# Kernel tuning notes

Measured on AMD Instinct MI355X. Metric: run time of the kernel, lower is better.

Reference implementation:

```python
import jax, jax.numpy as jnp
import numpy as np

NUM_HEADS = 12


def setup_inputs() -> dict:
    key = jax.random.key(0)
    k0, k1, k2 = jax.random.split(key, 3)
    B, N, C = 32, 864, 768  # N = 2*t_h*t_w + s_h*s_w = 288 + 576
    x = jax.random.normal(k0, (B, N, C), dtype=jnp.float32)
    W_qkv = jax.random.normal(k1, (C, 3 * C), dtype=jnp.float32) * 0.02
    W_proj = jax.random.normal(k2, (C, C), dtype=jnp.float32) * 0.02
    b_proj = jnp.zeros((C,), dtype=jnp.float32)
    return {"x": x, "W_qkv": W_qkv, "W_proj": W_proj, "b_proj": b_proj,
            "t_h": 12, "t_w": 12, "s_h": 24, "s_w": 24}


def reference(x, W_qkv, W_proj, b_proj, t_h, t_w, s_h, s_w):
    B, N, C = x.shape
    H = NUM_HEADS
    d = C // H
    scale = d ** -0.5
    # qkv projection (no bias), shape [3, B, H, N, d]
    qkv = (x @ W_qkv).reshape(B, N, 3, H, d).transpose(2, 0, 3, 1, 4)
    q, k, v = qkv[0], qkv[1], qkv[2]
    Tt = 2 * t_h * t_w            # temporal (template) query tokens = 288
    Ts = s_h * s_w                # spatial (search) query tokens = 576
    Mt = 2 * ((t_h + 1) // 2) ** 2  # sub-sampled temporal kv tokens = 72
    Ms = (s_h * s_w) // 4           # sub-sampled spatial kv tokens = 144
    q_t, q_s = q[:, :, :Tt], q[:, :, Tt:Tt + Ts]
    k_t, k_s = k[:, :, :Mt], k[:, :, Mt:Mt + Ms]
    v_t, v_s = v[:, :, :Mt], v[:, :, Mt:Mt + Ms]
    # temporal queries attend spatial keys/values
    a_t = jax.nn.softmax(jnp.einsum('bhqd,bhkd->bhqk', q_t, k_s) * scale, axis=-1)
    x_t = jnp.einsum('bhqk,bhkd->bhqd', a_t, v_s).transpose(0, 2, 1, 3).reshape(B, Tt, C)
    # spatial queries attend temporal keys/values
    a_s = jax.nn.softmax(jnp.einsum('bhqd,bhkd->bhqk', q_s, k_t) * scale, axis=-1)
    x_s = jnp.einsum('bhqk,bhkd->bhqd', a_s, v_t).transpose(0, 2, 1, 3).reshape(B, Ts, C)
    out = jnp.concatenate([x_t, x_s], axis=1)  # [B, N, C]
    return out @ W_proj + b_proj
```

## Files before the change

### kernel.cpp

```cpp
#include <hip/hip_runtime.h>
#include <hip/hip_bf16.h>

typedef __attribute__((ext_vector_type(8))) short short8;
typedef __attribute__((ext_vector_type(4))) float floatx4;

#define MFMA16(a, b, c) __builtin_amdgcn_mfma_f32_16x16x32_bf16((a), (b), (c), 0, 0, 0)

static constexpr int Bb = 32, Nn = 864, Cc = 768, Hh = 12;
static constexpr int Mm = Bb * Nn;
static constexpr int KVROWS = 256;

__device__ __forceinline__ void gload_lds16(const __hip_bfloat16* g, __hip_bfloat16* l) {
    __builtin_amdgcn_global_load_lds((const __attribute__((address_space(1))) void*)g,
                                     (__attribute__((address_space(3))) void*)l, 16, 0, 0);
}

static constexpr int CVT_BLKS = (Mm * Cc / 4) / 256;
static constexpr int TQKV_BLKS = (3 * Cc / 32) * (Cc / 32);
static constexpr int TPROJ_BLKS = (Cc / 32) * (Cc / 32);

__global__ __launch_bounds__(256) void prep_kernel(const float* __restrict__ x,
                                                   const float* __restrict__ Wqkv,
                                                   const float* __restrict__ Wproj,
                                                   __hip_bfloat16* __restrict__ xb,
                                                   __hip_bfloat16* __restrict__ WqkvT,
                                                   __hip_bfloat16* __restrict__ WprojT) {
    __shared__ float tile[32][33];
    const int bx = blockIdx.x;
    if (bx < CVT_BLKS) {
        const int i = bx * 256 + threadIdx.x;
        const float4 v = ((const float4*)x)[i];
        __hip_bfloat16 o[4] = {__float2bfloat16(v.x), __float2bfloat16(v.y),
                               __float2bfloat16(v.z), __float2bfloat16(v.w)};
        ((uint2*)xb)[i] = *(const uint2*)o;
        return;
    }
    const float* in;
    __hip_bfloat16* out;
    int R, C, bid;
    if (bx < CVT_BLKS + TQKV_BLKS) {
        bid = bx - CVT_BLKS; in = Wqkv; out = WqkvT; R = Cc; C = 3 * Cc;
    } else {
        bid = bx - CVT_BLKS - TQKV_BLKS; in = Wproj; out = WprojT; R = Cc; C = Cc;
    }
    const int c0 = (bid % (C / 32)) * 32, r0 = (bid / (C / 32)) * 32;
    const int tx = threadIdx.x & 31, ty = threadIdx.x >> 5;
#pragma unroll
    for (int i = 0; i < 32; i += 8)
        tile[ty + i][tx] = in[(size_t)(r0 + ty + i) * C + c0 + tx];
    __syncthreads();
#pragma unroll
    for (int i = 0; i < 32; i += 8)
        out[(size_t)(c0 + ty + i) * R + r0 + tx] = __float2bfloat16(tile[tx][ty + i]);
}

static constexpr int QBLKS = 6 * (Mm / 128);
static constexpr int KVBLKS = 12 * (Bb * KVROWS / 128);
static constexpr int QKV_NWG = QBLKS + KVBLKS;

__global__ __launch_bounds__(256) void gemm_qkv(const __hip_bfloat16* __restrict__ A,
                                                const __hip_bfloat16* __restrict__ WqkvT,
                                                __hip_bfloat16* __restrict__ Qbuf,
                                                __hip_bfloat16* __restrict__ Kbuf,
                                                __hip_bfloat16* __restrict__ VTbuf) {
    __shared__ __align__(16) char SMEM[32768];
    __hip_bfloat16* As = (__hip_bfloat16*)SMEM;
    __hip_bfloat16* Bs = As + 8192;

    const int braw = (int)blockIdx.x;
    const int sid = (braw & 7) * (QKV_NWG / 8) + (braw >> 3);

    int arow0, orow0, btrow, ncol0, bb = 0, keybase = 0;
    __hip_bfloat16* Out;
    int Nout;
    bool vmode = false;
    if (sid < QBLKS) {
        const int nt = sid % 6, mt = sid / 6;
        arow0 = mt * 128; orow0 = arow0;
        btrow = nt * 128; ncol0 = nt * 128;
        Out = Qbuf; Nout = Cc;
    } else {
        const int s = sid - QBLKS;
        const int nt = s % 12, mt = s / 12;
        bb = mt >> 1; keybase = (mt & 1) << 7;
        arow0 = bb * Nn + keybase;
        btrow = Cc + nt * 128;
        if (nt < 6) {
            orow0 = bb * KVROWS + keybase; ncol0 = nt * 128;
            Out = Kbuf; Nout = Cc;
        } else {
            vmode = true; ncol0 = (nt - 6) * 128;
            Out = nullptr; Nout = 0; orow0 = 0;
        }
    }

    const int t = threadIdx.x;
    const int lane = t & 63, wave = t >> 6;
    const int wm = (wave >> 1) * 64, wn = (wave & 1) * 64;
    const int ln = lane & 15, quad = lane >> 4;

    floatx4 acc[4][4] = {};

    const int r0 = t >> 2;
    const int cst = (t & 3) * 8;
    const __hip_bfloat16* Ag = A + (size_t)(arow0 + r0) * Cc + cst;
    const __hip_bfloat16* Bg = WqkvT + (size_t)(btrow + r0) * Cc + cst;
    const size_t rowskip = (size_t)64 * Cc;

    for (int k0 = 0; k0 < Cc; k0 += 64) {
        gload_lds16(Ag + k0,                &As[t * 8]);
        gload_lds16(Ag + k0 + rowskip,      &As[2048 + t * 8]);
        gload_lds16(Ag + k0 + 32,           &As[4096 + t * 8]);
        gload_lds16(Ag + k0 + 32 + rowskip, &As[6144 + t * 8]);
        gload_lds16(Bg + k0,                &Bs[t * 8]);
        gload_lds16(Bg + k0 + rowskip,      &Bs[2048 + t * 8]);
        gload_lds16(Bg + k0 + 32,           &Bs[4096 + t * 8]);
        gload_lds16(Bg + k0 + 32 + rowskip, &Bs[6144 + t * 8]);
        __syncthreads();

#pragma unroll
        for (int s = 0; s < 2; s++) {
            short8 af[4], bfr[4];
#pragma unroll
            for (int i = 0; i < 4; i++)
                af[i] = *(const short8*)&As[s * 4096 + (wm + i * 16 + ln) * 32 + quad * 8];
#pragma unroll
            for (int j = 0; j < 4; j++)
                bfr[j] = *(const short8*)&Bs[s * 4096 + (wn + j * 16 + ln) * 32 + quad * 8];
#pragma unroll
            for (int i = 0; i < 4; i++)
#pragma unroll
                for (int j = 0; j < 4; j++)
                    acc[i][j] = MFMA16(af[i], bfr[j], acc[i][j]);
        }
        __syncthreads();
    }

    if (!vmode) {
#pragma unroll
        for (int j = 0; j < 4; j++) {
            const int n = ncol0 + wn + j * 16 + ln;
#pragma unroll
            for (int i = 0; i < 4; i++) {
                const int mrow = orow0 + wm + i * 16 + quad * 4;
#pragma unroll
                for (int r = 0; r < 4; r++)
                    Out[(size_t)(mrow + r) * Nout + n] = __float2bfloat16(acc[i][j][r]);
            }
        }
        return;
    }

    __hip_bfloat16* T = (__hip_bfloat16*)SMEM;
#pragma unroll
    for (int pass = 0; pass < 2; pass++) {
        if ((wave & 1) == pass) {
#pragma unroll
            for (int j = 0; j < 4; j++) {
                const int ddl = j * 16 + ln;
#pragma unroll
                for (int i = 0; i < 4; i++) {
                    const int key = wm + i * 16 + quad * 4;
                    const __hip_bfloat162 lo =
                        __float22bfloat162_rn(make_float2(acc[i][j][0], acc[i][j][1]));
                    const __hip_bfloat162 hi =
                        __float22bfloat162_rn(make_float2(acc[i][j][2], acc[i][j][3]));
                    uint2 pk = make_uint2(*(const unsigned int*)&lo,
                                          *(const unsigned int*)&hi);
                    *(uint2*)&T[ddl * 136 + key] = pk;
                }
            }
        }
        __syncthreads();
#pragma unroll
        for (int it = 0; it < 4; it++) {
            const int ldd = it * 16 + (t >> 4);
            const int kk = (t & 15) * 8;
            const short8 v = *(const short8*)&T[ldd * 136 + kk];
            *(short8*)&VTbuf[(size_t)(bb * Cc + ncol0 + pass * 64 + ldd) * KVROWS +
                             keybase + kk] = v;
        }
        if (pass == 0) __syncthreads();
    }
}

__global__ __launch_bounds__(256) void gemm_proj(const __hip_bfloat16* __restrict__ A,
                                                 const __hip_bfloat16* __restrict__ BT,
                                                 float* __restrict__ Cout,
                                                 const float* __restrict__ bias) {
    __shared__ __align__(16) __hip_bfloat16 As[8192];
    __shared__ __align__(16) __hip_bfloat16 Bs[8192];
    const int gx = (int)gridDim.x;
    const int nwg = gx * (int)gridDim.y;
    const int braw = (int)blockIdx.y * gx + (int)blockIdx.x;
    const int sid = (braw & 7) * (nwg >> 3) + (braw >> 3);
    const int mt = sid / gx, nt = sid - mt * gx;
    const int m0 = mt << 7, n0 = nt * 128;
    const int t = threadIdx.x;
    const int lane = t & 63, wave = t >> 6;
    const int wm = (wave >> 1) * 64, wn = (wave & 1) * 64;
    const int ln = lane & 15, quad = lane >> 4;

    floatx4 acc[4][4] = {};
    const int r0 = t >> 2, cst = (t & 3) * 8;
    const __hip_bfloat16* Ag = A + (size_t)(m0 + r0) * Cc + cst;
    const __hip_bfloat16* Bg = BT + (size_t)(n0 + r0) * Cc + cst;
    const size_t rowskip = (size_t)64 * Cc;

    for (int k0 = 0; k0 < Cc; k0 += 64) {
        gload_lds16(Ag + k0,                &As[t * 8]);
        gload_lds16(Ag + k0 + rowskip,      &As[2048 + t * 8]);
        gload_lds16(Ag + k0 + 32,           &As[4096 + t * 8]);
        gload_lds16(Ag + k0 + 32 + rowskip, &As[6144 + t * 8]);
        gload_lds16(Bg + k0,                &Bs[t * 8]);
        gload_lds16(Bg + k0 + rowskip,      &Bs[2048 + t * 8]);
        gload_lds16(Bg + k0 + 32,           &Bs[4096 + t * 8]);
        gload_lds16(Bg + k0 + 32 + rowskip, &Bs[6144 + t * 8]);
        __syncthreads();
#pragma unroll
        for (int s = 0; s < 2; s++) {
            short8 af[4], bfr[4];
#pragma unroll
            for (int i = 0; i < 4; i++)
                af[i] = *(const short8*)&As[s * 4096 + (wm + i * 16 + ln) * 32 + quad * 8];
#pragma unroll
            for (int j = 0; j < 4; j++)
                bfr[j] = *(const short8*)&Bs[s * 4096 + (wn + j * 16 + ln) * 32 + quad * 8];
#pragma unroll
            for (int i = 0; i < 4; i++)
#pragma unroll
                for (int j = 0; j < 4; j++)
                    acc[i][j] = MFMA16(af[i], bfr[j], acc[i][j]);
        }
        __syncthreads();
    }
#pragma unroll
    for (int j = 0; j < 4; j++) {
        const int n = n0 + wn + j * 16 + ln;
        const float bv = bias[n];
#pragma unroll
        for (int i = 0; i < 4; i++) {
            const int mrow = m0 + wm + i * 16 + quad * 4;
#pragma unroll
            for (int r = 0; r < 4; r++)
                Cout[(size_t)(mrow + r) * Cc + n] = acc[i][j][r] + bv;
        }
    }
}

template <int L, int QOFF, int KVOFF, int NCH>
__device__ __forceinline__ void attn_pair(const __hip_bfloat16* __restrict__ qb,
                                          const __hip_bfloat16* __restrict__ kb,
                                          const __hip_bfloat16* __restrict__ vtb,
                                          __hip_bfloat16* __restrict__ attn,
                                          int p, int h, int b) {
    const int lane = threadIdx.x & 63;
    const int ln = lane & 15, quad = lane >> 4;

    const __hip_bfloat16* kbase = kb + (size_t)(b * KVROWS + KVOFF) * Cc + h * 64;
    const __hip_bfloat16* vtbase = vtb + (size_t)(b * Cc + h * 64) * KVROWS + KVOFF;

    const int qt0 = 2 * p;
    const __hip_bfloat16* qrowA =
        qb + (size_t)(b * Nn + QOFF + qt0 * 16 + ln) * Cc + h * 64;
    const __hip_bfloat16* qrowB = qrowA + (size_t)16 * Cc;
    const short8 aqA0 = *(const short8*)(qrowA + quad * 8);
    const short8 aqA1 = *(const short8*)(qrowA + 32 + quad * 8);
    const short8 aqB0 = *(const short8*)(qrowB + quad * 8);
    const short8 aqB1 = *(const short8*)(qrowB + 32 + quad * 8);

    float dsA = 0.0f, dsB = 0.0f;
    floatx4 accA[4] = {}, accB[4] = {};
    constexpr float CSC = 0.18033688011112042f;

#pragma unroll
    for (int ch = 0; ch < NCH; ch++) {
        unsigned int pkA[2][2] = {}, pkB[2][2] = {};
#pragma unroll
        for (int ti2 = 0; ti2 < 2; ti2++) {
            const int ti = ch * 2 + ti2;
            if (ti * 16 >= L) continue;
            const __hip_bfloat16* krow = kbase + (size_t)(ti * 16 + ln) * Cc;
            const short8 k0 = *(const short8*)(krow + quad * 8);
            const short8 k1 = *(const short8*)(krow + 32 + quad * 8);
            floatx4 sA = {0.f, 0.f, 0.f, 0.f}, sB = {0.f, 0.f, 0.f, 0.f};
            sA = MFMA16(k0, aqA0, sA);
            sA = MFMA16(k1, aqA1, sA);
            sB = MFMA16(k0, aqB0, sB);
            sB = MFMA16(k1, aqB1, sB);
            float pA[4], pB[4];
#pragma unroll
            for (int r = 0; r < 4; r++) {
                float eA = exp2f(sA[r] * CSC);
                float eB = exp2f(sB[r] * CSC);
                if (ti * 16 + 16 > L) {
                    if (ti * 16 + quad * 4 + r >= L) { eA = 0.0f; eB = 0.0f; }
                }
                pA[r] = eA; dsA += eA;
                pB[r] = eB; dsB += eB;
            }
            {
                const __hip_bfloat162 lo = __float22bfloat162_rn(make_float2(pA[0], pA[1]));
                const __hip_bfloat162 hi = __float22bfloat162_rn(make_float2(pA[2], pA[3]));
                pkA[ti2][0] = *(const unsigned int*)&lo;
                pkA[ti2][1] = *(const unsigned int*)&hi;
            }
            {
                const __hip_bfloat162 lo = __float22bfloat162_rn(make_float2(pB[0], pB[1]));
                const __hip_bfloat162 hi = __float22bfloat162_rn(make_float2(pB[2], pB[3]));
                pkB[ti2][0] = *(const unsigned int*)&lo;
                pkB[ti2][1] = *(const unsigned int*)&hi;
            }
        }
        const int srcA = ln + ((quad & 1) << 5);
        const int srcB = srcA + 16;
        const bool hi2 = quad >= 2;
        union { unsigned int u[4]; short8 v; } pfA, pfB;
        {
            const unsigned int c0 = (unsigned int)__shfl((int)pkA[0][0], srcA);
            const unsigned int c1 = (unsigned int)__shfl((int)pkA[0][1], srcA);
            const unsigned int c2 = (unsigned int)__shfl((int)pkA[0][0], srcB);
            const unsigned int c3 = (unsigned int)__shfl((int)pkA[0][1], srcB);
            const unsigned int d0 = (unsigned int)__shfl((int)pkA[1][0], srcA);
            const unsigned int d1 = (unsigned int)__shfl((int)pkA[1][1], srcA);
            const unsigned int d2 = (unsigned int)__shfl((int)pkA[1][0], srcB);
            const unsigned int d3 = (unsigned int)__shfl((int)pkA[1][1], srcB);
            pfA.u[0] = hi2 ? d0 : c0;
            pfA.u[1] = hi2 ? d1 : c1;
            pfA.u[2] = hi2 ? d2 : c2;
            pfA.u[3] = hi2 ? d3 : c3;
        }
        {
            const unsigned int c0 = (unsigned int)__shfl((int)pkB[0][0], srcA);
            const unsigned int c1 = (unsigned int)__shfl((int)pkB[0][1], srcA);
            const unsigned int c2 = (unsigned int)__shfl((int)pkB[0][0], srcB);
            const unsigned int c3 = (unsigned int)__shfl((int)pkB[0][1], srcB);
            const unsigned int d0 = (unsigned int)__shfl((int)pkB[1][0], srcA);
            const unsigned int d1 = (unsigned int)__shfl((int)pkB[1][1], srcA);
            const unsigned int d2 = (unsigned int)__shfl((int)pkB[1][0], srcB);
            const unsigned int d3 = (unsigned int)__shfl((int)pkB[1][1], srcB);
            pfB.u[0] = hi2 ? d0 : c0;
            pfB.u[1] = hi2 ? d1 : c1;
            pfB.u[2] = hi2 ? d2 : c2;
            pfB.u[3] = hi2 ? d3 : c3;
        }
#pragma unroll
        for (int j = 0; j < 4; j++) {
            const short8 vt =
                *(const short8*)&vtbase[(size_t)(j * 16 + ln) * KVROWS + ch * 32 + quad * 8];
            accA[j] = MFMA16(vt, pfA.v, accA[j]);
            accB[j] = MFMA16(vt, pfB.v, accB[j]);
        }
    }

    dsA += __shfl_xor(dsA, 16); dsA += __shfl_xor(dsA, 32);
    dsB += __shfl_xor(dsB, 16); dsB += __shfl_xor(dsB, 32);
    const float invA = 1.0f / dsA, invB = 1.0f / dsB;

    const size_t orowA = (size_t)(b * Nn + QOFF + qt0 * 16 + ln) * Cc + h * 64;
    const size_t orowB = orowA + (size_t)16 * Cc;
#pragma unroll
    for (int j = 0; j < 4; j++) {
        {
            const __hip_bfloat162 lo =
                __float22bfloat162_rn(make_float2(accA[j][0] * invA, accA[j][1] * invA));
            const __hip_bfloat162 hi =
                __float22bfloat162_rn(make_float2(accA[j][2] * invA, accA[j][3] * invA));
            uint2 o = make_uint2(*(const unsigned int*)&lo, *(const unsigned int*)&hi);
            *(uint2*)&attn[orowA + j * 16 + quad * 4] = o;
        }
        {
            const __hip_bfloat162 lo =
                __float22bfloat162_rn(make_float2(accB[j][0] * invB, accB[j][1] * invB));
            const __hip_bfloat162 hi =
                __float22bfloat162_rn(make_float2(accB[j][2] * invB, accB[j][3] * invB));
            uint2 o = make_uint2(*(const unsigned int*)&lo, *(const unsigned int*)&hi);
            *(uint2*)&attn[orowB + j * 16 + quad * 4] = o;
        }
    }
}

static constexpr int ATTN_BLKS = (384 * 27) / 4;

__global__ __launch_bounds__(256) void attn_fused(const __hip_bfloat16* __restrict__ qb,
                                                  const __hip_bfloat16* __restrict__ kb,
                                                  const __hip_bfloat16* __restrict__ vtb,
                                                  __hip_bfloat16* __restrict__ attn) {
    const int rid = (int)blockIdx.x;
    const int vid = (rid & 7) * (ATTN_BLKS / 8) + (rid >> 3);
    const int g = vid * 4 + (threadIdx.x >> 6);
    const int bh = g / 27, slot = g - bh * 27;
    const int h = bh % 12, b = bh / 12;
    if (slot < 9)
        attn_pair<144, 0, 72, 5>(qb, kb, vtb, attn, slot, h, b);
    else
        attn_pair<72, 288, 0, 3>(qb, kb, vtb, attn, slot - 9, h, b);
}

extern "C" void kernel_launch(void* const* d_in, const int* in_sizes, int n_in,
                              void* d_out, int out_size, void* d_ws, size_t ws_size,
                              hipStream_t stream) {
    const float* x     = (const float*)d_in[0];
    const float* Wqkv  = (const float*)d_in[1];
    const float* Wproj = (const float*)d_in[2];
    const float* bproj = (const float*)d_in[3];
    float* out = (float*)d_out;

    char* ws = (char*)d_ws;
    __hip_bfloat16* xb     = (__hip_bfloat16*)ws;
    __hip_bfloat16* WqkvT  = (__hip_bfloat16*)(ws + 42467328);
    __hip_bfloat16* WprojT = (__hip_bfloat16*)(ws + 46006272);
    __hip_bfloat16* Qbuf   = (__hip_bfloat16*)(ws + 47185920);
    __hip_bfloat16* Kbuf   = (__hip_bfloat16*)(ws + 89653248);
    __hip_bfloat16* VTbuf  = (__hip_bfloat16*)(ws + 102236160);
    __hip_bfloat16* attn   = (__hip_bfloat16*)ws;

    prep_kernel<<<CVT_BLKS + TQKV_BLKS + TPROJ_BLKS, 256, 0, stream>>>(x, Wqkv, Wproj, xb,
                                                                       WqkvT, WprojT);
    gemm_qkv<<<QKV_NWG, 256, 0, stream>>>(xb, WqkvT, Qbuf, Kbuf, VTbuf);
    attn_fused<<<ATTN_BLKS, 256, 0, stream>>>(Qbuf, Kbuf, VTbuf, attn);
    gemm_proj<<<dim3(Cc / 128, Mm / 128), 256, 0, stream>>>(attn, WprojT, out, bproj);
}
```

Before: 345.0 us.

## Stage V-transpose tile in LDS per (batch,head) block, one query tile per wave

The attention kernel now gives each block a single (batch, head) pair plus a chunk of query tiles. The block cooperatively loads that head's transposed V slice into LDS with a rotated, padded layout to avoid bank conflicts, and each wave then processes one 16-row query tile instead of two. This replaces repeated uncoalesced global V reads with LDS reads, but adds a barrier and an LDS footprint, and some waves exit idle in the last chunk. Both the QKV GEMM and the attention kernel also get a minimum-occupancy launch bound of 5, which may constrain register allocation.

```diff
diff --git a/kernel.cpp b/kernel.cpp
--- a/kernel.cpp
+++ b/kernel.cpp
@@ -58,11 +58,11 @@
 static constexpr int KVBLKS = 12 * (Bb * KVROWS / 128);
 static constexpr int QKV_NWG = QBLKS + KVBLKS;
 
-__global__ __launch_bounds__(256) void gemm_qkv(const __hip_bfloat16* __restrict__ A,
-                                                const __hip_bfloat16* __restrict__ WqkvT,
-                                                __hip_bfloat16* __restrict__ Qbuf,
-                                                __hip_bfloat16* __restrict__ Kbuf,
-                                                __hip_bfloat16* __restrict__ VTbuf) {
+__global__ __launch_bounds__(256, 5) void gemm_qkv(const __hip_bfloat16* __restrict__ A,
+                                                   const __hip_bfloat16* __restrict__ WqkvT,
+                                                   __hip_bfloat16* __restrict__ Qbuf,
+                                                   __hip_bfloat16* __restrict__ Kbuf,
+                                                   __hip_bfloat16* __restrict__ VTbuf) {
     __shared__ __align__(16) char SMEM[32768];
     __hip_bfloat16* As = (__hip_bfloat16*)SMEM;
     __hip_bfloat16* Bs = As + 8192;
@@ -248,153 +248,133 @@
     }
 }
 
-template <int L, int QOFF, int KVOFF, int NCH>
-__device__ __forceinline__ void attn_pair(const __hip_bfloat16* __restrict__ qb,
+template <int L, int QOFF, int KVOFF, int NQT, int NCH>
+__device__ __forceinline__ void attn_part(const __hip_bfloat16* __restrict__ qb,
                                           const __hip_bfloat16* __restrict__ kb,
                                           const __hip_bfloat16* __restrict__ vtb,
                                           __hip_bfloat16* __restrict__ attn,
-                                          int p, int h, int b) {
-    const int lane = threadIdx.x & 63;
+                                          int qc, int h, int b,
+                                          __hip_bfloat16* VTs) {
+    constexpr int KPAD = NCH * 32;
+    constexpr int NB8 = KPAD / 8;
+    constexpr int VSTR = KPAD + 8;
+    const int t = threadIdx.x, lane = t & 63;
     const int ln = lane & 15, quad = lane >> 4;
 
     const __hip_bfloat16* kbase = kb + (size_t)(b * KVROWS + KVOFF) * Cc + h * 64;
-    const __hip_bfloat16* vtbase = vtb + (size_t)(b * Cc + h * 64) * KVROWS + KVOFF;
-
-    const int qt0 = 2 * p;
-    const __hip_bfloat16* qrowA =
-        qb + (size_t)(b * Nn + QOFF + qt0 * 16 + ln) * Cc + h * 64;
-    const __hip_bfloat16* qrowB = qrowA + (size_t)16 * Cc;
-    const short8 aqA0 = *(const short8*)(qrowA + quad * 8);
-    const short8 aqA1 = *(const short8*)(qrowA + 32 + quad * 8);
-    const short8 aqB0 = *(const short8*)(qrowB + quad * 8);
-    const short8 aqB1 = *(const short8*)(qrowB + 32 + quad * 8);
-
-    float dsA = 0.0f, dsB = 0.0f;
-    floatx4 accA[4] = {}, accB[4] = {};
+    const __hip_bfloat16* vtbase =
+        vtb + (size_t)(b * Cc + h * 64) * KVROWS + KVOFF;
+
+    for (int c = t; c < 64 * NB8; c += 256) {
+        const int dd = c / NB8, kbk = c - dd * NB8;
+        const int colp8 = (kbk + dd) % NB8;
+        uint4 val = make_uint4(0u, 0u, 0u, 0u);
+        if (kbk * 8 < L)
+            val = *(const uint4*)(vtbase + (size_t)dd * KVROWS + kbk * 8);
+        *(uint4*)&VTs[dd * VSTR + colp8 * 8] = val;
+    }
+    __syncthreads();
+
+    const int qt = qc * 4 + (t >> 6);
+    if (qt >= NQT) return;
+
+    const __hip_bfloat16* qrow = qb + (size_t)(b * Nn + QOFF + qt * 16 + ln) * Cc + h * 64;
+    const short8 aq0 = *(const short8*)(qrow + quad * 8);
+    const short8 aq1 = *(const short8*)(qrow + 32 + quad * 8);
+
+    int ddm[4];
+#pragma unroll
+    for (int j = 0; j < 4; j++) ddm[j] = (j * 16 + ln) % NB8;
+
+    float dsum = 0.0f;
+    floatx4 acco[4] = {};
     constexpr float CSC = 0.18033688011112042f;
 
 #pragma unroll
     for (int ch = 0; ch < NCH; ch++) {
-        unsigned int pkA[2][2] = {}, pkB[2][2] = {};
+        unsigned int pk[2][2];
 #pragma unroll
         for (int ti2 = 0; ti2 < 2; ti2++) {
             const int ti = ch * 2 + ti2;
-            if (ti * 16 >= L) continue;
+            if (ti * 16 >= L) {
+                pk[ti2][0] = 0u; pk[ti2][1] = 0u;
+                continue;
+            }
             const __hip_bfloat16* krow = kbase + (size_t)(ti * 16 + ln) * Cc;
             const short8 k0 = *(const short8*)(krow + quad * 8);
             const short8 k1 = *(const short8*)(krow + 32 + quad * 8);
-            floatx4 sA = {0.f, 0.f, 0.f, 0.f}, sB = {0.f, 0.f, 0.f, 0.f};
-            sA = MFMA16(k0, aqA0, sA);
-            sA = MFMA16(k1, aqA1, sA);
-            sB = MFMA16(k0, aqB0, sB);
-            sB = MFMA16(k1, aqB1, sB);
-            float pA[4], pB[4];
+            floatx4 s = {0.f, 0.f, 0.f, 0.f};
+            s = MFMA16(k0, aq0, s);
+            s = MFMA16(k1, aq1, s);
+            float p[4];
 #pragma unroll
             for (int r = 0; r < 4; r++) {
-                float eA = exp2f(sA[r] * CSC);
-                float eB = exp2f(sB[r] * CSC);
-                if (ti * 16 + 16 > L) {
-                    if (ti * 16 + quad * 4 + r >= L) { eA = 0.0f; eB = 0.0f; }
-                }
-                pA[r] = eA; dsA += eA;
-                pB[r] = eB; dsB += eB;
+                float e = exp2f(s[r] * CSC);
+                if (ti * 16 + 16 > L)
+                    if (ti * 16 + quad * 4 + r >= L) e = 0.0f;
+                p[r] = e;
+                dsum += e;
             }
-            {
-                const __hip_bfloat162 lo = __float22bfloat162_rn(make_float2(pA[0], pA[1]));
-                const __hip_bfloat162 hi = __float22bfloat162_rn(make_float2(pA[2], pA[3]));
-                pkA[ti2][0] = *(const unsigned int*)&lo;
-                pkA[ti2][1] = *(const unsigned int*)&hi;
-            }
-            {
-                const __hip_bfloat162 lo = __float22bfloat162_rn(make_float2(pB[0], pB[1]));
-                const __hip_bfloat162 hi = __float22bfloat162_rn(make_float2(pB[2], pB[3]));
-                pkB[ti2][0] = *(const unsigned int*)&lo;
-                pkB[ti2][1] = *(const unsigned int*)&hi;
-            }
+            const __hip_bfloat162 lo = __float22bfloat162_rn(make_float2(p[0], p[1]));
+            const __hip_bfloat162 hi = __float22bfloat162_rn(make_float2(p[2], p[3]));
+            pk[ti2][0] = *(const unsigned int*)&lo;
+            pk[ti2][1] = *(const unsigned int*)&hi;
         }
         const int srcA = ln + ((quad & 1) << 5);
         const int srcB = srcA + 16;
+        const unsigned int c0 = (unsigned int)__shfl((int)pk[0][0], srcA);
+        const unsigned int c1 = (unsigned int)__shfl((int)pk[0][1], srcA);
+        const unsigned int c2 = (unsigned int)__shfl((int)pk[0][0], srcB);
+        const unsigned int c3 = (unsigned int)__shfl((int)pk[0][1], srcB);
+        const unsigned int d0 = (unsigned int)__shfl((int)pk[1][0], srcA);
+        const unsigned int d1 = (unsigned int)__shfl((int)pk[1][1], srcA);
+        const unsigned int d2 = (unsigned int)__shfl((int)pk[1][0], srcB);
+        const unsigned int d3 = (unsigned int)__shfl((int)pk[1][1], srcB);
         const bool hi2 = quad >= 2;
-        union { unsigned int u[4]; short8 v; } pfA, pfB;
-        {
-            const unsigned int c0 = (unsigned int)__shfl((int)pkA[0][0], srcA);
-            const unsigned int c1 = (unsigned int)__shfl((int)pkA[0][1], srcA);
-            const unsigned int c2 = (unsigned int)__shfl((int)pkA[0][0], srcB);
-            const unsigned int c3 = (unsigned int)__shfl((int)pkA[0][1], srcB);
-            const unsigned int d0 = (unsigned int)__shfl((int)pkA[1][0], srcA);
-            const unsigned int d1 = (unsigned int)__shfl((int)pkA[1][1], srcA);
-            const unsigned int d2 = (unsigned int)__shfl((int)pkA[1][0], srcB);
-            const unsigned int d3 = (unsigned int)__shfl((int)pkA[1][1], srcB);
-            pfA.u[0] = hi2 ? d0 : c0;
-            pfA.u[1] = hi2 ? d1 : c1;
-            pfA.u[2] = hi2 ? d2 : c2;
-            pfA.u[3] = hi2 ? d3 : c3;
-        }
-        {
-            const unsigned int c0 = (unsigned int)__shfl((int)pkB[0][0], srcA);
-            const unsigned int c1 = (unsigned int)__shfl((int)pkB[0][1], srcA);
-            const unsigned int c2 = (unsigned int)__shfl((int)pkB[0][0], srcB);
-            const unsigned int c3 = (unsigned int)__shfl((int)pkB[0][1], srcB);
-            const unsigned int d0 = (unsigned int)__shfl((int)pkB[1][0], srcA);
-            const unsigned int d1 = (unsigned int)__shfl((int)pkB[1][1], srcA);
-            const unsigned int d2 = (unsigned int)__shfl((int)pkB[1][0], srcB);
-            const unsigned int d3 = (unsigned int)__shfl((int)pkB[1][1], srcB);
-            pfB.u[0] = hi2 ? d0 : c0;
-            pfB.u[1] = hi2 ? d1 : c1;
-            pfB.u[2] = hi2 ? d2 : c2;
-            pfB.u[3] = hi2 ? d3 : c3;
-        }
+        union { unsigned int u[4]; short8 v; } pf;
+        pf.u[0] = hi2 ? d0 : c0;
+        pf.u[1] = hi2 ? d1 : c1;
+        pf.u[2] = hi2 ? d2 : c2;
+        pf.u[3] = hi2 ? d3 : c3;
 #pragma unroll
         for (int j = 0; j < 4; j++) {
-            const short8 vt =
-                *(const short8*)&vtbase[(size_t)(j * 16 + ln) * KVROWS + ch * 32 + quad * 8];
-            accA[j] = MFMA16(vt, pfA.v, accA[j]);
-            accB[j] = MFMA16(vt, pfB.v, accB[j]);
-        }
-    }
-
-    dsA += __shfl_xor(dsA, 16); dsA += __shfl_xor(dsA, 32);
-    dsB += __shfl_xor(dsB, 16); dsB += __shfl_xor(dsB, 32);
-    const float invA = 1.0f / dsA, invB = 1.0f / dsB;
-
-    const size_t orowA = (size_t)(b * Nn + QOFF + qt0 * 16 + ln) * Cc + h * 64;
-    const size_t orowB = orowA + (size_t)16 * Cc;
+            int cb = ch * 4 + quad + ddm[j];
+            if (cb >= NB8) cb -= NB8;
+            const short8 vt = *(const short8*)&VTs[(j * 16 + ln) * VSTR + cb * 8];
+            acco[j] = MFMA16(vt, pf.v, acco[j]);
+        }
+    }
+
+    dsum += __shfl_xor(dsum, 16);
+    dsum += __shfl_xor(dsum, 32);
+    const float inv = 1.0f / dsum;
+
+    const size_t orow = (size_t)(b * Nn + QOFF + qt * 16 + ln) * Cc + h * 64;
 #pragma unroll
     for (int j = 0; j < 4; j++) {
-        {
-            const __hip_bfloat162 lo =
-                __float22bfloat162_rn(make_float2(accA[j][0] * invA, accA[j][1] * invA));
-            const __hip_bfloat162 hi =
-                __float22bfloat162_rn(make_float2(accA[j][2] * invA, accA[j][3] * invA));
-            uint2 o = make_uint2(*(const unsigned int*)&lo, *(const unsigned int*)&hi);
-            *(uint2*)&attn[orowA + j * 16 + quad * 4] = o;
-        }
-        {
-            const __hip_bfloat162 lo =
-                __float22bfloat162_rn(make_float2(accB[j][0] * invB, accB[j][1] * invB));
-            const __hip_bfloat162 hi =
-                __float22bfloat162_rn(make_float2(accB[j][2] * invB, accB[j][3] * invB));
-            uint2 o = make_uint2(*(const unsigned int*)&lo, *(const unsigned int*)&hi);
-            *(uint2*)&attn[orowB + j * 16 + quad * 4] = o;
-        }
-    }
-}
-
-static constexpr int ATTN_BLKS = (384 * 27) / 4;
-
-__global__ __launch_bounds__(256) void attn_fused(const __hip_bfloat16* __restrict__ qb,
-                                                  const __hip_bfloat16* __restrict__ kb,
-                                                  const __hip_bfloat16* __restrict__ vtb,
-                                                  __hip_bfloat16* __restrict__ attn) {
-    const int rid = (int)blockIdx.x;
-    const int vid = (rid & 7) * (ATTN_BLKS / 8) + (rid >> 3);
-    const int g = vid * 4 + (threadIdx.x >> 6);
-    const int bh = g / 27, slot = g - bh * 27;
-    const int h = bh % 12, b = bh / 12;
-    if (slot < 9)
-        attn_pair<144, 0, 72, 5>(qb, kb, vtb, attn, slot, h, b);
+        const __hip_bfloat162 lo =
+            __float22bfloat162_rn(make_float2(acco[j][0] * inv, acco[j][1] * inv));
+        const __hip_bfloat162 hi =
+            __float22bfloat162_rn(make_float2(acco[j][2] * inv, acco[j][3] * inv));
+        uint2 o = make_uint2(*(const unsigned int*)&lo, *(const unsigned int*)&hi);
+        *(uint2*)&attn[orow + j * 16 + quad * 4] = o;
+    }
+}
+
+__global__ __launch_bounds__(256, 5) void attn_fused(const __hip_bfloat16* __restrict__ qb,
+                                                     const __hip_bfloat16* __restrict__ kb,
+                                                     const __hip_bfloat16* __restrict__ vtb,
+                                                     __hip_bfloat16* __restrict__ attn) {
+    __shared__ __align__(16) __hip_bfloat16 VTs[64 * 168];
+    constexpr int NB = 14 * 12 * 32;
+    const int rid = (int)blockIdx.x + 14 * ((int)blockIdx.y + 12 * (int)blockIdx.z);
+    const int vid = (rid & 7) * (NB / 8) + (rid >> 3);
+    const int qc = vid % 14, g = vid / 14;
+    const int h = g % 12, bq = g / 12;
+    if (qc < 5)
+        attn_part<144, 0, 72, 18, 5>(qb, kb, vtb, attn, qc, h, bq, VTs);
     else
-        attn_pair<72, 288, 0, 3>(qb, kb, vtb, attn, slot - 9, h, b);
+        attn_part<72, 288, 0, 36, 3>(qb, kb, vtb, attn, qc - 5, h, bq, VTs);
 }
 
 extern "C" void kernel_launch(void* const* d_in, const int* in_sizes, int n_in,
@@ -418,6 +398,6 @@
     prep_kernel<<<CVT_BLKS + TQKV_BLKS + TPROJ_BLKS, 256, 0, stream>>>(x, Wqkv, Wproj, xb,
                                                                        WqkvT, WprojT);
     gemm_qkv<<<QKV_NWG, 256, 0, stream>>>(xb, WqkvT, Qbuf, Kbuf, VTbuf);
-    attn_fused<<<ATTN_BLKS, 256, 0, stream>>>(Qbuf, Kbuf, VTbuf, attn);
+    attn_fused<<<dim3(14, Hh, Bb), 256, 0, stream>>>(Qbuf, Kbuf, VTbuf, attn);
     gemm_proj<<<dim3(Cc / 128, Mm / 128), 256, 0, stream>>>(attn, WprojT, out, bproj);
 }
```

Result: slower. 360.4 us (+4.5%).
